# Kernel tuning notes

Measured on AMD Instinct MI355X. Metric: run time of the kernel, lower is better.

Reference implementation:

```python
import jax, jax.numpy as jnp
import numpy as np

HEADS = 8
DIM_HEAD = 64
SCALE = DIM_HEAD ** -0.5


def setup_inputs() -> dict:
    key = jax.random.key(0)
    ks = jax.random.split(key, 6)
    b, n, t, d, cond_dim, hidden = 2, 8, 1024, 512, 512, HEADS * DIM_HEAD
    return {
        "x": jax.random.normal(ks[0], (b * n, t, d), dtype=jnp.float32),
        "label_emb_mm": jax.random.normal(ks[1], (b, n, cond_dim), dtype=jnp.float32),
        "Wqkv": jax.random.normal(ks[2], (d, 3 * hidden), dtype=jnp.float32) * (d ** -0.5),
        "Wk": jax.random.normal(ks[3], (cond_dim, hidden), dtype=jnp.float32) * (cond_dim ** -0.5),
        "Wv": jax.random.normal(ks[4], (cond_dim, hidden), dtype=jnp.float32) * (cond_dim ** -0.5),
        "Wout": jax.random.normal(ks[5], (hidden, d), dtype=jnp.float32) * (hidden ** -0.5),
        "b": 2,
    }


def reference(x, label_emb_mm, Wqkv, Wk, Wv, Wout, b):
    bn, t, d = x.shape
    n = bn // b
    h, dh = HEADS, DIM_HEAD
    xb = x.reshape(b, n, t, d)
    # fused QKV projection: (b, n, t, 3*h*dh)
    qkv = xb @ Wqkv
    q, k, v = jnp.split(qkv, 3, axis=-1)

    def to_heads(z):  # (b, n, t, h*dh) -> (b, n, h, t, dh)
        return z.reshape(b, n, t, h, dh).transpose(0, 1, 3, 2, 4)

    q, k, v = to_heads(q), to_heads(k), to_heads(v)
    # per-frame conditioning K/V: one extra token per frame
    ek = (label_emb_mm @ Wk).reshape(b, n, 1, h, dh).transpose(0, 1, 3, 2, 4)
    ev = (label_emb_mm @ Wv).reshape(b, n, 1, h, dh).transpose(0, 1, 3, 2, 4)
    k = jnp.concatenate([ek, k], axis=-2)  # (b, n, h, 1+t, dh)
    v = jnp.concatenate([ev, v], axis=-2)
    q = q * SCALE
    sim = jnp.einsum("bnhid,bnhjd->bnhij", q, k)
    attn = jax.nn.softmax(sim, axis=-1)
    out = jnp.einsum("bnhij,bnhjd->bnhid", attn, v)
    out = out.transpose(0, 1, 3, 2, 4).reshape(b, n, t, h * dh)
    out = out @ Wout
    return out.reshape(b * n, t, d)
```

## Files before the change

kernel.cpp:

```cpp
#include <hip/hip_runtime.h>
#include <stdint.h>

typedef unsigned short u16;
typedef __bf16 bf16x8 __attribute__((ext_vector_type(8)));
typedef float f32x4 __attribute__((ext_vector_type(4)));
typedef float f32x16 __attribute__((ext_vector_type(16)));

__device__ __forceinline__ u16 f2bf(float f) {
  uint32_t u = __builtin_bit_cast(uint32_t, f);
  u += 0x7FFFu + ((u >> 16) & 1u);
  return (u16)(u >> 16);
}
__device__ __forceinline__ float bf2f(u16 v) {
  return __builtin_bit_cast(float, ((uint32_t)v) << 16);
}

#if __has_builtin(__builtin_amdgcn_exp2f)
__device__ __forceinline__ float exp2_fast(float x) { return __builtin_amdgcn_exp2f(x); }
#else
__device__ __forceinline__ float exp2_fast(float x) { return exp2f(x); }
#endif

__device__ __forceinline__ void gload_lds16(const u16* g, u16* l) {
  __builtin_amdgcn_global_load_lds(
      (const __attribute__((address_space(1))) uint32_t*)g,
      (__attribute__((address_space(3))) uint32_t*)l, 16, 0, 0);
}

__device__ __forceinline__ uint32_t cvtpk(float lo, float hi) {
  uint32_t r;
  asm("v_cvt_pk_bf16_f32 %0, %1, %2" : "=v"(r) : "v"(lo), "v"(hi));
  return r;
}
__device__ __forceinline__ void plswap(uint32_t& a, uint32_t& b) {
  asm volatile("v_permlane32_swap_b32 %0, %1" : "+v"(a), "+v"(b));
}

__global__ __launch_bounds__(256) void prep_kernel(
    const float* __restrict__ x, const float* __restrict__ Wqkv,
    const float* __restrict__ Wout, const float* __restrict__ label,
    const float* __restrict__ Wk, const float* __restrict__ Wv,
    u16* __restrict__ xb, u16* __restrict__ WqkvT, u16* __restrict__ WoutT,
    u16* __restrict__ ek, u16* __restrict__ ev, float qscale) {
  const int b = blockIdx.x;
  if (b < 4096) {
    int i = (b * 256 + threadIdx.x) * 8;
    float4 a = *(const float4*)(x + i);
    float4 c = *(const float4*)(x + i + 4);
    union { u16 u[8]; uint4 v; } r;
    r.u[0] = f2bf(a.x); r.u[1] = f2bf(a.y); r.u[2] = f2bf(a.z); r.u[3] = f2bf(a.w);
    r.u[4] = f2bf(c.x); r.u[5] = f2bf(c.y); r.u[6] = f2bf(c.z); r.u[7] = f2bf(c.w);
    *(uint4*)(xb + i) = r.v;
  } else if (b < 7168) {
    int id = (b - 4096) * 256 + threadIdx.x;
    int k = id & 511, nn = id >> 9;
    float v = Wqkv[(size_t)k * 1536 + nn];
    if (nn < 512) v *= qscale;
    WqkvT[id] = f2bf(v);
  } else if (b < 8192) {
    int id = (b - 7168) * 256 + threadIdx.x;
    int k = id & 511, nn = id >> 9;
    WoutT[id] = f2bf(Wout[(size_t)k * 512 + nn]);
  } else {
    __shared__ float sdata[256];
    const int bb = b - 8192;
    const int chunk = bb & 7, row = (bb >> 3) & 15;
    const float* W = (bb & 128) ? Wv : Wk;
    u16* o = (bb & 128) ? ev : ek;
    const int tid = threadIdx.x;
    const int col = chunk * 64 + (tid & 63);
    const int ks = tid >> 6;
    const float* lr = label + row * 512 + ks * 128;
    const float* wp = W + (size_t)(ks * 128) * 512 + col;
    float acc = 0.f;
#pragma unroll 8
    for (int i = 0; i < 128; ++i)
      acc = fmaf(lr[i], wp[(size_t)i * 512], acc);
    sdata[tid] = acc;
    __syncthreads();
    if (tid < 64) {
      float t = sdata[tid] + sdata[tid + 64] + sdata[tid + 128] + sdata[tid + 192];
      o[row * 512 + chunk * 64 + tid] = f2bf(t);
    }
  }
}

template <int MODE>
__global__ __launch_bounds__(512, 2) void gemm_bt_kernel(
    const u16* __restrict__ A, const u16* __restrict__ B,
    u16* __restrict__ OQ, u16* __restrict__ OKb, u16* __restrict__ OVT,
    float* __restrict__ OF, int K, int N) {
  constexpr int BN = (MODE == 0) ? 192 : 128;
  constexpr int NI = BN / 64;
  constexpr int NRB = BN / 64;
  constexpr int NBY = (MODE == 0) ? 8 : 4;
  constexpr int VM = 4 + NRB;

  __shared__ __align__(16) u16 As[2][256 * 64];
  __shared__ __align__(16) u16 Bs[2][BN * 64];

  const int tid = threadIdx.x;
  const int w = tid >> 6, lane = tid & 63;
  const int l15 = lane & 15, lg = lane >> 4;
  const int wr = w >> 2, wc = w & 3;

  const int q8 = gridDim.x >> 3;
  const int wg = (blockIdx.x & 7) * q8 + (blockIdx.x >> 3);
  const int bx = wg / NBY, by = wg % NBY;

  const int srow = tid >> 3, schunk = tid & 7;
  const u16* Ag = A + (size_t)(bx * 256 + srow) * K + ((schunk ^ (srow & 7)) * 8);
  const u16* Bg = B + (size_t)(by * BN + srow) * K + ((schunk ^ (srow & 7)) * 8);

  int aoff[8][2], boff[NI][2];
#pragma unroll
  for (int mi = 0; mi < 8; ++mi)
#pragma unroll
    for (int ks = 0; ks < 2; ++ks) {
      const int row = wr * 128 + mi * 16 + l15;
      aoff[mi][ks] = row * 64 + (((ks * 4 + lg) ^ (row & 7)) * 8);
    }
#pragma unroll
  for (int ni = 0; ni < NI; ++ni)
#pragma unroll
    for (int ks = 0; ks < 2; ++ks) {
      const int row = wc * (BN / 4) + ni * 16 + l15;
      boff[ni][ks] = row * 64 + (((ks * 4 + lg) ^ (row & 7)) * 8);
    }

  f32x4 acc[8][NI] = {};

  const int nt = K >> 6;
#define STAGE(buf, k0)                                                       \
  {                                                                          \
    _Pragma("unroll") for (int ra = 0; ra < 4; ++ra)                         \
        gload_lds16(Ag + (k0) + (size_t)(ra * 64) * K,                       \
                    &As[buf][(ra * 64 + w * 8) * 64]);                       \
    _Pragma("unroll") for (int rb = 0; rb < NRB; ++rb)                       \
        gload_lds16(Bg + (k0) + (size_t)(rb * 64) * K,                       \
                    &Bs[buf][(rb * 64 + w * 8) * 64]);                       \
  }
#define COMPUTE(cb)                                                          \
  {                                                                          \
    const u16* Ab = &As[cb][0];                                              \
    const u16* Bb = &Bs[cb][0];                                              \
    _Pragma("unroll") for (int ks = 0; ks < 2; ++ks) {                       \
      bf16x8 a[8], b[NI];                                                    \
      _Pragma("unroll") for (int mi = 0; mi < 8; ++mi)                       \
          a[mi] = *(const bf16x8*)&Ab[aoff[mi][ks]];                         \
      _Pragma("unroll") for (int ni = 0; ni < NI; ++ni)                      \
          b[ni] = *(const bf16x8*)&Bb[boff[ni][ks]];                         \
      __builtin_amdgcn_s_setprio(1);                                         \
      _Pragma("unroll") for (int mi = 0; mi < 8; ++mi)                       \
          _Pragma("unroll") for (int ni = 0; ni < NI; ++ni)                  \
              acc[mi][ni] = __builtin_amdgcn_mfma_f32_16x16x32_bf16(          \
                  a[mi], b[ni], acc[mi][ni], 0, 0, 0);                       \
      __builtin_amdgcn_s_setprio(0);                                         \
    }                                                                        \
  }

  STAGE(0, 0);
  STAGE(1, 64);

  for (int t = 0; t < nt - 1; ++t) {
    if constexpr (VM == 7)
      asm volatile("s_waitcnt vmcnt(7)" ::: "memory");
    else
      asm volatile("s_waitcnt vmcnt(6)" ::: "memory");
    __builtin_amdgcn_s_barrier();
    __builtin_amdgcn_sched_barrier(0);
    COMPUTE(t & 1);
    if (t + 2 < nt) {
      __builtin_amdgcn_s_barrier();
      __builtin_amdgcn_sched_barrier(0);
      STAGE(t & 1, (t + 2) * 64);
    }
  }
  asm volatile("s_waitcnt vmcnt(0)" ::: "memory");
  __builtin_amdgcn_s_barrier();
  __builtin_amdgcn_sched_barrier(0);
  COMPUTE((nt - 1) & 1);
#undef STAGE
#undef COMPUTE

  const int row0 = bx * 256 + wr * 128 + lg * 4;
  if constexpr (MODE == 1) {
#pragma unroll
    for (int mi = 0; mi < 8; ++mi)
#pragma unroll
      for (int ni = 0; ni < NI; ++ni) {
        int col = by * BN + wc * (BN / 4) + ni * 16 + l15;
#pragma unroll
        for (int r = 0; r < 4; ++r)
          OF[(size_t)(row0 + mi * 16 + r) * N + col] = acc[mi][ni][r];
      }
  } else {
#pragma unroll
    for (int mi = 0; mi < 8; ++mi)
#pragma unroll
      for (int ni = 0; ni < NI; ++ni) {
        const int gcol = by * BN + wc * (BN / 4) + ni * 16 + l15;
        const int sect = gcol >> 9;
        const int colL = gcol & 511;
        if (sect < 2) {
          u16* O = sect ? OKb : OQ;
#pragma unroll
          for (int r = 0; r < 4; ++r)
            O[(size_t)(row0 + mi * 16 + r) * 512 + colL] = f2bf(acc[mi][ni][r]);
        } else {
          int h = colL >> 6, dh = colL & 63;
          int rr = row0 + mi * 16;
          int bn = rr >> 10, t0 = rr & 1023;
          ushort4 pk;
          pk.x = f2bf(acc[mi][ni][0]);
          pk.y = f2bf(acc[mi][ni][1]);
          pk.z = f2bf(acc[mi][ni][2]);
          pk.w = f2bf(acc[mi][ni][3]);
          *(ushort4*)&OVT[(size_t)((bn * 8 + h) * 64 + dh) * 1024 + t0] = pk;
        }
      }
  }
}

__global__ __launch_bounds__(256, 4) void attn_kernel(
    const u16* __restrict__ Qb, const u16* __restrict__ Kb, const u16* __restrict__ VTb,
    const u16* __restrict__ ekb, const u16* __restrict__ evb, u16* __restrict__ Ob) {
  __shared__ __align__(16) u16 Kl[64 * 64];
  __shared__ __align__(16) u16 Vl[64 * 64];

  const int tid = threadIdx.x;
  const int w = tid >> 6, lane = tid & 63;
  const int l31 = lane & 31, hi = lane >> 5;
  const int lb = (blockIdx.x & 7) * 128 + (blockIdx.x >> 3);
  const int head = lb >> 3, qt = lb & 7;
  const int bn = head >> 3, h = head & 7;
  const int q0 = qt * 128 + w * 32;

  const int srow = lane >> 3;
  const int schunk = (lane & 7) ^ srow;
  const u16* Kg0 = Kb + (size_t)(bn * 1024 + w * 16 + srow) * 512 + h * 64 + schunk * 8;
  const u16* Vg0 = VTb + (size_t)(head * 64 + w * 16 + srow) * 1024 + schunk * 8;
  u16* KlDst = &Kl[w * 1024];
  u16* VlDst = &Vl[w * 1024];

  bf16x8 qf[4];
#pragma unroll
  for (int c = 0; c < 4; ++c)
    qf[c] = *(const bf16x8*)(Qb + (size_t)(bn * 1024 + q0 + l31) * 512 +
                             h * 64 + c * 16 + hi * 8);

  bf16x8 bones1;
  {
    union { u16 u[8]; bf16x8 v; } ob;
#pragma unroll
    for (int j = 0; j < 8; ++j) ob.u[j] = (u16)0x3F80;
    bones1 = ob.v;
  }

  f32x16 acc[2];
  f32x16 acc5;
  {
    float dot = 0.f;
#pragma unroll
    for (int c = 0; c < 4; ++c) {
      bf16x8 ekf = *(const bf16x8*)(ekb + bn * 512 + h * 64 + c * 16 + hi * 8);
#pragma unroll
      for (int j = 0; j < 8; ++j)
        dot += (float)qf[c][j] * (float)ekf[j];
    }
    uint32_t a = __builtin_bit_cast(uint32_t, dot), b = a;
    plswap(a, b);
    float part = (lane < 32) ? __builtin_bit_cast(float, b) : __builtin_bit_cast(float, a);
    float pe = exp2_fast(dot + part);

    union { u16 u[8]; bf16x8 v; } pef, evf[2];
#pragma unroll
    for (int j = 0; j < 8; ++j) pef.u[j] = 0;
    if (hi == 0) pef.u[0] = f2bf(pe);
#pragma unroll
    for (int dt = 0; dt < 2; ++dt) {
#pragma unroll
      for (int j = 0; j < 8; ++j) evf[dt].u[j] = 0;
      if (hi == 0) evf[dt].u[0] = evb[bn * 512 + h * 64 + dt * 32 + l31];
    }
    f32x16 z = {};
#pragma unroll
    for (int dt = 0; dt < 2; ++dt)
      acc[dt] = __builtin_amdgcn_mfma_f32_32x32x16_bf16(pef.v, evf[dt].v, z, 0, 0, 0);
    acc5 = __builtin_amdgcn_mfma_f32_32x32x16_bf16(pef.v, bones1, z, 0, 0, 0);
  }

  for (int jt = 0; jt < 16; ++jt) {
    const int j0 = jt * 64;
    __syncthreads();
    gload_lds16(Kg0 + (size_t)j0 * 512, KlDst);
    gload_lds16(Kg0 + (size_t)(j0 + 8) * 512, KlDst + 512);
    gload_lds16(Vg0 + j0, VlDst);
    gload_lds16(Vg0 + j0 + (size_t)8 * 1024, VlDst + 512);
    __syncthreads();

#pragma unroll
    for (int sub = 0; sub < 2; ++sub) {
      const int rk = sub * 32 + l31;
      bf16x8 kb[4];
#pragma unroll
      for (int c = 0; c < 4; ++c)
        kb[c] = *(const bf16x8*)&Kl[rk * 64 + (((c * 2 + hi) ^ (rk & 7)) * 8)];

      f32x16 s = {};
#pragma unroll
      for (int c = 0; c < 4; ++c)
        s = __builtin_amdgcn_mfma_f32_32x32x16_bf16(kb[c], qf[c], s, 0, 0, 0);

      uint32_t wd[8];
#pragma unroll
      for (int i = 0; i < 8; ++i)
        wd[i] = cvtpk(exp2_fast(s[2 * i]), exp2_fast(s[2 * i + 1]));
      plswap(wd[0], wd[2]);
      plswap(wd[1], wd[3]);
      plswap(wd[4], wd[6]);
      plswap(wd[5], wd[7]);
      union { uint32_t w[4]; bf16x8 v; } f0, f1;
      f0.w[0] = wd[0]; f0.w[1] = wd[1]; f0.w[2] = wd[2]; f0.w[3] = wd[3];
      f1.w[0] = wd[4]; f1.w[1] = wd[5]; f1.w[2] = wd[6]; f1.w[3] = wd[7];
      bf16x8 pa0 = f0.v, pa1 = f1.v;

#pragma unroll
      for (int dt = 0; dt < 2; ++dt) {
        const int rv = dt * 32 + l31;
        bf16x8 vb0 = *(const bf16x8*)&Vl[rv * 64 + (((sub * 4 + hi) ^ (rv & 7)) * 8)];
        acc[dt] = __builtin_amdgcn_mfma_f32_32x32x16_bf16(pa0, vb0, acc[dt], 0, 0, 0);
        bf16x8 vb1 = *(const bf16x8*)&Vl[rv * 64 + (((sub * 4 + 2 + hi) ^ (rv & 7)) * 8)];
        acc[dt] = __builtin_amdgcn_mfma_f32_32x32x16_bf16(pa1, vb1, acc[dt], 0, 0, 0);
      }
      acc5 = __builtin_amdgcn_mfma_f32_32x32x16_bf16(pa0, bones1, acc5, 0, 0, 0);
      acc5 = __builtin_amdgcn_mfma_f32_32x32x16_bf16(pa1, bones1, acc5, 0, 0, 0);
    }
  }

#pragma unroll
  for (int r = 0; r < 16; ++r) {
    const float inv = 1.0f / acc5[r];
    const int q = q0 + (r & 3) + 8 * (r >> 2) + 4 * hi;
    u16* op = Ob + (size_t)(bn * 1024 + q) * 512 + h * 64 + l31;
    op[0] = f2bf(acc[0][r] * inv);
    op[32] = f2bf(acc[1][r] * inv);
  }
}

extern "C" void kernel_launch(void* const* d_in, const int* in_sizes, int n_in,
                              void* d_out, int out_size, void* d_ws, size_t ws_size,
                              hipStream_t stream) {
  (void)in_sizes; (void)n_in; (void)out_size; (void)ws_size;
  const float* x     = (const float*)d_in[0];
  const float* label = (const float*)d_in[1];
  const float* Wqkv  = (const float*)d_in[2];
  const float* Wk    = (const float*)d_in[3];
  const float* Wv    = (const float*)d_in[4];
  const float* Wout  = (const float*)d_in[5];
  float* out = (float*)d_out;

  char* ws = (char*)d_ws;
  u16* xb    = (u16*)(ws);
  u16* WqkvT = (u16*)(ws + 16777216);
  u16* WoutT = (u16*)(ws + 18350080);
  u16* ekb   = (u16*)(ws + 18874368);
  u16* evb   = (u16*)(ws + 18890752);
  u16* Qbuf  = (u16*)(ws + 18907136);
  u16* Kbuf  = (u16*)(ws + 35684352);
  u16* VTbuf = (u16*)(ws + 52461568);

  const float qscale = 0.125f * 1.4426950408889634f;

  prep_kernel<<<8448, 256, 0, stream>>>(x, Wqkv, Wout, label, Wk, Wv,
                                        xb, WqkvT, WoutT, ekb, evb, qscale);

  gemm_bt_kernel<0><<<512, 512, 0, stream>>>(xb, WqkvT, Qbuf, Kbuf, VTbuf, nullptr, 512, 1536);

  attn_kernel<<<1024, 256, 0, stream>>>(Qbuf, Kbuf, VTbuf, ekb, evb, xb);

  gemm_bt_kernel<1><<<256, 512, 0, stream>>>(xb, WoutT, nullptr, nullptr, nullptr, out, 512, 512);
}
```

Measured before the change: 123.1 us.

## Double-buffer K/V tiles and give each wave two query subtiles in attention

Attention kernel now uses 2 waves per block, each owning 64 query rows (two 32-row subtiles) so every K tile loaded from LDS is reused across two QK^T MFMAs. K/V tiles are double-buffered with the next tile prefetched while the current one is computed, which removes one barrier per iteration. The softmax denominator is now accumulated with scalar adds plus a cross-lane reduction instead of extra MFMAs against a ones vector, and MFMA sections are wrapped in s_setprio. The cost is higher register pressure and fewer waves per block, which may reduce occupancy and latency hiding.

```diff
diff --git a/kernel.cpp b/kernel.cpp
--- a/kernel.cpp
+++ b/kernel.cpp
@@ -222,11 +222,11 @@
   }
 }
 
-__global__ __launch_bounds__(256, 4) void attn_kernel(
+__global__ __launch_bounds__(128, 2) void attn_kernel(
     const u16* __restrict__ Qb, const u16* __restrict__ Kb, const u16* __restrict__ VTb,
     const u16* __restrict__ ekb, const u16* __restrict__ evb, u16* __restrict__ Ob) {
-  __shared__ __align__(16) u16 Kl[64 * 64];
-  __shared__ __align__(16) u16 Vl[64 * 64];
+  __shared__ __align__(16) u16 Kl[2][64 * 64];
+  __shared__ __align__(16) u16 Vl[2][64 * 64];
 
   const int tid = threadIdx.x;
   const int w = tid >> 6, lane = tid & 63;
@@ -234,70 +234,78 @@
   const int lb = (blockIdx.x & 7) * 128 + (blockIdx.x >> 3);
   const int head = lb >> 3, qt = lb & 7;
   const int bn = head >> 3, h = head & 7;
-  const int q0 = qt * 128 + w * 32;
+  const int q0 = qt * 128 + w * 64;
 
   const int srow = lane >> 3;
-  const int schunk = (lane & 7) ^ srow;
-  const u16* Kg0 = Kb + (size_t)(bn * 1024 + w * 16 + srow) * 512 + h * 64 + schunk * 8;
-  const u16* Vg0 = VTb + (size_t)(head * 64 + w * 16 + srow) * 1024 + schunk * 8;
-  u16* KlDst = &Kl[w * 1024];
-  u16* VlDst = &Vl[w * 1024];
-
-  bf16x8 qf[4];
-#pragma unroll
-  for (int c = 0; c < 4; ++c)
-    qf[c] = *(const bf16x8*)(Qb + (size_t)(bn * 1024 + q0 + l31) * 512 +
-                             h * 64 + c * 16 + hi * 8);
-
-  bf16x8 bones1;
+  const int schunk = lane & 7;
+  const u16* Kg0 = Kb + (size_t)(bn * 1024 + w * 32 + srow) * 512 + h * 64;
+  const u16* Vg0 = VTb + (size_t)(head * 64 + w * 32 + srow) * 1024;
+  int scol[4];
+#pragma unroll
+  for (int i = 0; i < 4; ++i)
+    scol[i] = ((schunk ^ ((w * 32 + i * 8 + srow) & 7)) * 8);
+
+#define STAGE(buf, j0)                                                        \
+  {                                                                           \
+    _Pragma("unroll") for (int i = 0; i < 4; ++i)                             \
+        gload_lds16(Kg0 + (size_t)((j0) + i * 8) * 512 + scol[i],             \
+                    &Kl[buf][(w * 32 + i * 8) * 64]);                         \
+    _Pragma("unroll") for (int i = 0; i < 4; ++i)                             \
+        gload_lds16(Vg0 + (j0) + (size_t)(i * 8) * 1024 + scol[i],            \
+                    &Vl[buf][(w * 32 + i * 8) * 64]);                         \
+  }
+
+  STAGE(0, 0);
+
+  bf16x8 qf[2][4];
+#pragma unroll
+  for (int qs = 0; qs < 2; ++qs)
+#pragma unroll
+    for (int c = 0; c < 4; ++c)
+      qf[qs][c] = *(const bf16x8*)(Qb + (size_t)(bn * 1024 + q0 + qs * 32 + l31) * 512 +
+                                   h * 64 + c * 16 + hi * 8);
+
+  f32x16 acc[2][2];
+  float psum[2];
   {
-    union { u16 u[8]; bf16x8 v; } ob;
-#pragma unroll
-    for (int j = 0; j < 8; ++j) ob.u[j] = (u16)0x3F80;
-    bones1 = ob.v;
-  }
-
-  f32x16 acc[2];
-  f32x16 acc5;
-  {
-    float dot = 0.f;
-#pragma unroll
-    for (int c = 0; c < 4; ++c) {
-      bf16x8 ekf = *(const bf16x8*)(ekb + bn * 512 + h * 64 + c * 16 + hi * 8);
-#pragma unroll
-      for (int j = 0; j < 8; ++j)
-        dot += (float)qf[c][j] * (float)ekf[j];
-    }
-    uint32_t a = __builtin_bit_cast(uint32_t, dot), b = a;
-    plswap(a, b);
-    float part = (lane < 32) ? __builtin_bit_cast(float, b) : __builtin_bit_cast(float, a);
-    float pe = exp2_fast(dot + part);
-
-    union { u16 u[8]; bf16x8 v; } pef, evf[2];
-#pragma unroll
-    for (int j = 0; j < 8; ++j) pef.u[j] = 0;
-    if (hi == 0) pef.u[0] = f2bf(pe);
-#pragma unroll
-    for (int dt = 0; dt < 2; ++dt) {
-#pragma unroll
-      for (int j = 0; j < 8; ++j) evf[dt].u[j] = 0;
-      if (hi == 0) evf[dt].u[0] = evb[bn * 512 + h * 64 + dt * 32 + l31];
-    }
-    f32x16 z = {};
-#pragma unroll
-    for (int dt = 0; dt < 2; ++dt)
-      acc[dt] = __builtin_amdgcn_mfma_f32_32x32x16_bf16(pef.v, evf[dt].v, z, 0, 0, 0);
-    acc5 = __builtin_amdgcn_mfma_f32_32x32x16_bf16(pef.v, bones1, z, 0, 0, 0);
-  }
+#pragma unroll
+    for (int qs = 0; qs < 2; ++qs) {
+      float dot = 0.f;
+#pragma unroll
+      for (int c = 0; c < 4; ++c) {
+        bf16x8 ekf = *(const bf16x8*)(ekb + bn * 512 + h * 64 + c * 16 + hi * 8);
+#pragma unroll
+        for (int j = 0; j < 8; ++j)
+          dot += (float)qf[qs][c][j] * (float)ekf[j];
+      }
+      uint32_t a = __builtin_bit_cast(uint32_t, dot), b = a;
+      plswap(a, b);
+      float part = (lane < 32) ? __builtin_bit_cast(float, b) : __builtin_bit_cast(float, a);
+      float pe = exp2_fast(dot + part);
+      psum[qs] = (hi == 0) ? pe : 0.f;
+
+      union { u16 u[8]; bf16x8 v; } pef, evf[2];
+#pragma unroll
+      for (int j = 0; j < 8; ++j) pef.u[j] = 0;
+      if (hi == 0) pef.u[0] = f2bf(pe);
+#pragma unroll
+      for (int dt = 0; dt < 2; ++dt) {
+#pragma unroll
+        for (int j = 0; j < 8; ++j) evf[dt].u[j] = 0;
+        if (hi == 0) evf[dt].u[0] = evb[bn * 512 + h * 64 + dt * 32 + l31];
+      }
+      f32x16 z = {};
+#pragma unroll
+      for (int dt = 0; dt < 2; ++dt)
+        acc[qs][dt] = __builtin_amdgcn_mfma_f32_32x32x16_bf16(pef.v, evf[dt].v, z, 0, 0, 0);
+    }
+  }
+
+  __syncthreads();
 
   for (int jt = 0; jt < 16; ++jt) {
-    const int j0 = jt * 64;
-    __syncthreads();
-    gload_lds16(Kg0 + (size_t)j0 * 512, KlDst);
-    gload_lds16(Kg0 + (size_t)(j0 + 8) * 512, KlDst + 512);
-    gload_lds16(Vg0 + j0, VlDst);
-    gload_lds16(Vg0 + j0 + (size_t)8 * 1024, VlDst + 512);
-    __syncthreads();
+    const int buf = jt & 1;
+    if (jt < 15) STAGE(buf ^ 1, (jt + 1) * 64);
 
 #pragma unroll
     for (int sub = 0; sub < 2; ++sub) {
@@ -305,46 +313,77 @@
       bf16x8 kb[4];
 #pragma unroll
       for (int c = 0; c < 4; ++c)
-        kb[c] = *(const bf16x8*)&Kl[rk * 64 + (((c * 2 + hi) ^ (rk & 7)) * 8)];
-
-      f32x16 s = {};
-#pragma unroll
-      for (int c = 0; c < 4; ++c)
-        s = __builtin_amdgcn_mfma_f32_32x32x16_bf16(kb[c], qf[c], s, 0, 0, 0);
-
-      uint32_t wd[8];
-#pragma unroll
-      for (int i = 0; i < 8; ++i)
-        wd[i] = cvtpk(exp2_fast(s[2 * i]), exp2_fast(s[2 * i + 1]));
-      plswap(wd[0], wd[2]);
-      plswap(wd[1], wd[3]);
-      plswap(wd[4], wd[6]);
-      plswap(wd[5], wd[7]);
-      union { uint32_t w[4]; bf16x8 v; } f0, f1;
-      f0.w[0] = wd[0]; f0.w[1] = wd[1]; f0.w[2] = wd[2]; f0.w[3] = wd[3];
-      f1.w[0] = wd[4]; f1.w[1] = wd[5]; f1.w[2] = wd[6]; f1.w[3] = wd[7];
-      bf16x8 pa0 = f0.v, pa1 = f1.v;
+        kb[c] = *(const bf16x8*)&Kl[buf][rk * 64 + (((c * 2 + hi) ^ (rk & 7)) * 8)];
+
+      f32x16 s[2] = {};
+      __builtin_amdgcn_s_setprio(1);
+#pragma unroll
+      for (int c = 0; c < 4; ++c) {
+        s[0] = __builtin_amdgcn_mfma_f32_32x32x16_bf16(kb[c], qf[0][c], s[0], 0, 0, 0);
+        s[1] = __builtin_amdgcn_mfma_f32_32x32x16_bf16(kb[c], qf[1][c], s[1], 0, 0, 0);
+      }
+      __builtin_amdgcn_s_setprio(0);
+
+      bf16x8 pa[2][2];
+#pragma unroll
+      for (int qs = 0; qs < 2; ++qs) {
+        uint32_t wd[8];
+        float ps0 = 0.f, ps1 = 0.f;
+#pragma unroll
+        for (int i = 0; i < 8; ++i) {
+          float e0 = exp2_fast(s[qs][2 * i]);
+          float e1 = exp2_fast(s[qs][2 * i + 1]);
+          ps0 += e0;
+          ps1 += e1;
+          wd[i] = cvtpk(e0, e1);
+        }
+        psum[qs] += ps0 + ps1;
+        plswap(wd[0], wd[2]);
+        plswap(wd[1], wd[3]);
+        plswap(wd[4], wd[6]);
+        plswap(wd[5], wd[7]);
+        union { uint32_t w[4]; bf16x8 v; } f0, f1;
+        f0.w[0] = wd[0]; f0.w[1] = wd[1]; f0.w[2] = wd[2]; f0.w[3] = wd[3];
+        f1.w[0] = wd[4]; f1.w[1] = wd[5]; f1.w[2] = wd[6]; f1.w[3] = wd[7];
+        pa[qs][0] = f0.v;
+        pa[qs][1] = f1.v;
+      }
 
 #pragma unroll
       for (int dt = 0; dt < 2; ++dt) {
         const int rv = dt * 32 + l31;
-        bf16x8 vb0 = *(const bf16x8*)&Vl[rv * 64 + (((sub * 4 + hi) ^ (rv & 7)) * 8)];
-        acc[dt] = __builtin_amdgcn_mfma_f32_32x32x16_bf16(pa0, vb0, acc[dt], 0, 0, 0);
-        bf16x8 vb1 = *(const bf16x8*)&Vl[rv * 64 + (((sub * 4 + 2 + hi) ^ (rv & 7)) * 8)];
-        acc[dt] = __builtin_amdgcn_mfma_f32_32x32x16_bf16(pa1, vb1, acc[dt], 0, 0, 0);
-      }
-      acc5 = __builtin_amdgcn_mfma_f32_32x32x16_bf16(pa0, bones1, acc5, 0, 0, 0);
-      acc5 = __builtin_amdgcn_mfma_f32_32x32x16_bf16(pa1, bones1, acc5, 0, 0, 0);
-    }
-  }
-
-#pragma unroll
-  for (int r = 0; r < 16; ++r) {
-    const float inv = 1.0f / acc5[r];
-    const int q = q0 + (r & 3) + 8 * (r >> 2) + 4 * hi;
-    u16* op = Ob + (size_t)(bn * 1024 + q) * 512 + h * 64 + l31;
-    op[0] = f2bf(acc[0][r] * inv);
-    op[32] = f2bf(acc[1][r] * inv);
+        bf16x8 vb0 = *(const bf16x8*)&Vl[buf][rv * 64 + (((sub * 4 + hi) ^ (rv & 7)) * 8)];
+        bf16x8 vb1 = *(const bf16x8*)&Vl[buf][rv * 64 + (((sub * 4 + 2 + hi) ^ (rv & 7)) * 8)];
+        __builtin_amdgcn_s_setprio(1);
+#pragma unroll
+        for (int qs = 0; qs < 2; ++qs) {
+          acc[qs][dt] = __builtin_amdgcn_mfma_f32_32x32x16_bf16(pa[qs][0], vb0, acc[qs][dt], 0, 0, 0);
+          acc[qs][dt] = __builtin_amdgcn_mfma_f32_32x32x16_bf16(pa[qs][1], vb1, acc[qs][dt], 0, 0, 0);
+        }
+        __builtin_amdgcn_s_setprio(0);
+      }
+    }
+
+    __syncthreads();
+  }
+#undef STAGE
+
+#pragma unroll
+  for (int qs = 0; qs < 2; ++qs) {
+    uint32_t a = __builtin_bit_cast(uint32_t, psum[qs]), b = a;
+    plswap(a, b);
+    float other = (lane < 32) ? __builtin_bit_cast(float, b) : __builtin_bit_cast(float, a);
+    float lsum = psum[qs] + other;
+#pragma unroll
+    for (int r = 0; r < 16; ++r) {
+      const int qloc = (r & 3) + 8 * (r >> 2) + 4 * hi;
+      const float ls = __shfl(lsum, qloc);
+      const float inv = 1.0f / ls;
+      const int q = q0 + qs * 32 + qloc;
+      u16* op = Ob + (size_t)(bn * 1024 + q) * 512 + h * 64 + l31;
+      op[0] = f2bf(acc[qs][0][r] * inv);
+      op[32] = f2bf(acc[qs][1][r] * inv);
+    }
   }
 }
 
@@ -377,7 +416,7 @@
 
   gemm_bt_kernel<0><<<512, 512, 0, stream>>>(xb, WqkvT, Qbuf, Kbuf, VTbuf, nullptr, 512, 1536);
 
-  attn_kernel<<<1024, 256, 0, stream>>>(Qbuf, Kbuf, VTbuf, ekb, evb, xb);
+  attn_kernel<<<1024, 128, 0, stream>>>(Qbuf, Kbuf, VTbuf, ekb, evb, xb);
 
   gemm_bt_kernel<1><<<256, 512, 0, stream>>>(xb, WoutT, nullptr, nullptr, nullptr, out, 512, 512);
 }
```

After: 124.4 us. No clear change (+1.1%).
